# Kernel tuning notes

Measured on AMD Instinct MI355X. Metric: run time of the kernel, lower is better.

The kernel has to match this reference:

```python
import jax, jax.numpy as jnp
import numpy as np
import math

INPUT_SIZE = 1024
OUTPUT_SIZE = 1024
QK_SIZE = 1024
B, S = 4, 2048


def setup_inputs() -> dict:
    key = jax.random.key(0)
    ks = jax.random.split(key, 7)
    scale = 1.0 / math.sqrt(INPUT_SIZE)
    return {
        "x": jax.random.normal(ks[0], (B, S, INPUT_SIZE), dtype=jnp.float32),
        "Wq": jax.random.uniform(ks[1], (QK_SIZE, INPUT_SIZE), minval=-scale, maxval=scale, dtype=jnp.float32),
        "bq": jax.random.uniform(ks[2], (QK_SIZE,), minval=-scale, maxval=scale, dtype=jnp.float32),
        "Wk": jax.random.uniform(ks[3], (QK_SIZE, INPUT_SIZE), minval=-scale, maxval=scale, dtype=jnp.float32),
        "bk": jax.random.uniform(ks[4], (QK_SIZE,), minval=-scale, maxval=scale, dtype=jnp.float32),
        "Wv": jax.random.uniform(ks[5], (OUTPUT_SIZE, INPUT_SIZE), minval=-scale, maxval=scale, dtype=jnp.float32),
        "bv": jax.random.uniform(ks[6], (OUTPUT_SIZE,), minval=-scale, maxval=scale, dtype=jnp.float32),
    }


def reference(x, Wq, bq, Wk, bk, Wv, bv):
    # torch Linear: y = x @ W.T + b
    q = jnp.einsum('bsd,ed->bse', x, Wq) + bq  # [B,S,QK]
    k = jnp.einsum('bsd,ed->bse', x, Wk) + bk  # [B,S,QK]
    v = jnp.einsum('bsd,ed->bse', x, Wv) + bv  # [B,S,OUT]
    inv_sqrt_d = 1.0 / math.sqrt(QK_SIZE)
    scores = jnp.einsum('bqe,bke->bqk', q, k) * inv_sqrt_d  # [B,S,S]
    attn = jax.nn.softmax(scores, axis=-1)
    return jnp.einsum('bqk,bko->bqo', attn, v)  # [B,S,OUT]
```

## Files before the change

kernel.cpp:

```cpp
#include <hip/hip_runtime.h>
#include <stdint.h>

typedef unsigned short u16;
typedef __attribute__((ext_vector_type(8))) __bf16 bf16x8;
typedef __attribute__((ext_vector_type(4))) float f32x4;

__device__ __forceinline__ u16 f2bf(float f) {
    union { float f; uint32_t u; } v; v.f = f;
    uint32_t r = (v.u + 0x7FFFu + ((v.u >> 16) & 1u)) >> 16;
    return (u16)r;
}

__device__ __forceinline__ void lds_fence() {
    __asm__ volatile("s_waitcnt lgkmcnt(0)" ::: "memory");
}

#define BM 128
#define BN 128
#define BK 64

template<int MODE>
__global__ __launch_bounds__(256, 4) void gemm_bt(
    const u16* __restrict__ A, const u16* __restrict__ Bt,
    const float* __restrict__ b0, const float* __restrict__ b1, const float* __restrict__ b2,
    u16* __restrict__ o0, u16* __restrict__ o1, u16* __restrict__ o2,
    float* __restrict__ o3, float* __restrict__ lsum,
    int M, int N, int K, long sA, long sB, long sC, float scale)
{
    __shared__ __align__(16) u16 smem[4 * 64 * 72];

    const int t = threadIdx.x;
    const int lane = t & 63;
    const int wave = t >> 6;
    const int wm = (wave & 1) * 64;
    const int wn = (wave >> 1) * 64;

    const int id = blockIdx.x;
    const int xcd = id & 7;
    const int s = id >> 3;
    int bm, bn;
    long bz;
    if (MODE == 0) {
        bn = (s >> 3) * BN;
        bm = (xcd * 8 + (s & 7)) * BM;
        bz = 0;
    } else if (MODE == 2) {
        bz = xcd >> 1;
        bn = (s & 15) * BN;
        bm = ((xcd & 1) * 8 + (s >> 4)) * BM;
    } else {
        bz = xcd >> 1;
        bn = (s & 7) * BN;
        bm = ((xcd & 1) * 8 + (s >> 3)) * BM;
    }

    const u16* Ab = A + bz * sA;
    const u16* Bb = Bt + bz * sB;

    f32x4 acc[4][4];
#pragma unroll
    for (int i = 0; i < 4; ++i)
#pragma unroll
        for (int j = 0; j < 4; ++j)
            acc[i][j] = (f32x4){0.f, 0.f, 0.f, 0.f};

    const int lrow = t >> 2;
    const int lcol = (t & 3) * 8;
    const int fm = lane & 15;
    const int fk = (lane >> 4) * 8;

    for (int k0 = 0; k0 < K; k0 += BK) {
#pragma unroll
        for (int h = 0; h < 2; ++h)
#pragma unroll
            for (int r = 0; r < 2; ++r) {
                const u16* ga = Ab + (long)(bm + r * 64 + lrow) * K + (k0 + h * 32 + lcol);
                __builtin_amdgcn_global_load_lds(
                    (const __attribute__((address_space(1))) void*)ga,
                    (__attribute__((address_space(3))) void*)&smem[h * 4096 + (r * 256 + t) * 8],
                    16, 0, 0);
            }
#pragma unroll
        for (int h = 0; h < 2; ++h)
#pragma unroll
            for (int r = 0; r < 2; ++r) {
                const u16* gb = Bb + (long)(bn + r * 64 + lrow) * K + (k0 + h * 32 + lcol);
                __builtin_amdgcn_global_load_lds(
                    (const __attribute__((address_space(1))) void*)gb,
                    (__attribute__((address_space(3))) void*)&smem[8192 + h * 4096 + (r * 256 + t) * 8],
                    16, 0, 0);
            }
        __syncthreads();

#pragma unroll
        for (int h = 0; h < 2; ++h) {
            bf16x8 af[4], bfr[4];
#pragma unroll
            for (int i = 0; i < 4; ++i) {
                af[i]  = *(const bf16x8*)&smem[h * 4096 + (wm + i * 16 + fm) * 32 + fk];
                bfr[i] = *(const bf16x8*)&smem[8192 + h * 4096 + (wn + i * 16 + fm) * 32 + fk];
            }
#pragma unroll
            for (int i = 0; i < 4; ++i)
#pragma unroll
                for (int j = 0; j < 4; ++j)
                    acc[i][j] = __builtin_amdgcn_mfma_f32_16x16x32_bf16(af[i], bfr[j], acc[i][j], 0, 0, 0);
        }
        __syncthreads();
    }

    const int cm = (lane >> 4) * 4;
    const int cn = lane & 15;
    u16* Ew = smem + wave * 4608;

    if (MODE == 3) {
        float* Fw = (float*)Ew;
#pragma unroll
        for (int p = 0; p < 2; ++p) {
            if (p) lds_fence();
#pragma unroll
            for (int ii = 0; ii < 2; ++ii) {
                const int i = p * 2 + ii;
#pragma unroll
                for (int j = 0; j < 4; ++j)
#pragma unroll
                    for (int r = 0; r < 4; ++r)
                        Fw[(ii * 16 + cm + r) * 68 + j * 16 + cn] = acc[i][j][r];
            }
#pragma unroll
            for (int it = 0; it < 8; ++it) {
                const int row = it * 4 + (lane >> 4);
                const int c4 = (lane & 15) * 4;
                f32x4 w = *(const f32x4*)&Fw[row * 68 + c4];
                const int gm = bm + wm + p * 32 + row;
                const float inv = __builtin_amdgcn_rcpf(lsum[bz * 2048 + gm]);
                w[0] *= inv; w[1] *= inv; w[2] *= inv; w[3] *= inv;
                *(f32x4*)&o3[bz * sC + (long)gm * N + bn + wn + c4] = w;
            }
        }
    } else if (MODE == 0 && (bn >> 10) == 2) {
        float bb[4];
#pragma unroll
        for (int j = 0; j < 4; ++j) bb[j] = b2[(bn & 1023) + wn + j * 16 + cn];
        const int bgi = (bm + wm) >> 11;
        const int sbase = (bm + wm) & 2047;
#pragma unroll
        for (int i = 0; i < 4; ++i)
#pragma unroll
            for (int j = 0; j < 4; ++j) {
                ushort4 pk;
                pk.x = f2bf(acc[i][j][0] + bb[j]);
                pk.y = f2bf(acc[i][j][1] + bb[j]);
                pk.z = f2bf(acc[i][j][2] + bb[j]);
                pk.w = f2bf(acc[i][j][3] + bb[j]);
                *(ushort4*)&Ew[(j * 16 + cn) * 72 + i * 16 + cm] = pk;
            }
#pragma unroll
        for (int it = 0; it < 8; ++it) {
            const int e = it * 8 + (lane >> 3);
            const int s8 = (lane & 7) * 8;
            const uint4 w = *(const uint4*)&Ew[e * 72 + s8];
            const int eg = (bn & 1023) + wn + e;
            *(uint4*)&o2[((((long)bgi << 10) + eg) << 11) + sbase + s8] = w;
        }
    } else if (MODE == 0) {
        const int sec = bn >> 10;
        u16* C = sec ? o1 : o0;
        const float* bias = sec ? b1 : b0;
        const int ncol0 = bn & 1023;
        float bb[4];
#pragma unroll
        for (int j = 0; j < 4; ++j) bb[j] = bias[ncol0 + wn + j * 16 + cn];
#pragma unroll
        for (int i = 0; i < 4; ++i)
#pragma unroll
            for (int j = 0; j < 4; ++j) {
                const int col = j * 16 + cn;
#pragma unroll
                for (int r = 0; r < 4; ++r)
                    Ew[(i * 16 + cm + r) * 72 + col] = f2bf(acc[i][j][r] + bb[j]);
            }
#pragma unroll
        for (int it = 0; it < 8; ++it) {
            const int row = it * 8 + (lane >> 3);
            const int c8 = (lane & 7) * 8;
            const uint4 w = *(const uint4*)&Ew[row * 72 + c8];
            const int gm = bm + wm + row;
            *(uint4*)&C[(long)gm * 1024 + ncol0 + wn + c8] = w;
        }
    } else {
#pragma unroll
        for (int i = 0; i < 4; ++i)
#pragma unroll
            for (int j = 0; j < 4; ++j)
#pragma unroll
                for (int r = 0; r < 4; ++r)
                    acc[i][j][r] = __expf(acc[i][j][r] * scale);
#pragma unroll
        for (int i = 0; i < 4; ++i) {
#pragma unroll
            for (int r = 0; r < 4; ++r) {
                float sm = acc[i][0][r] + acc[i][1][r] + acc[i][2][r] + acc[i][3][r];
                sm += __shfl_xor(sm, 1);
                sm += __shfl_xor(sm, 2);
                sm += __shfl_xor(sm, 4);
                sm += __shfl_xor(sm, 8);
                if (cn == 0)
                    atomicAdd(&lsum[bz * 2048 + bm + wm + i * 16 + cm + r], sm);
            }
        }
#pragma unroll
        for (int i = 0; i < 4; ++i)
#pragma unroll
            for (int j = 0; j < 4; ++j) {
                const int col = j * 16 + cn;
#pragma unroll
                for (int r = 0; r < 4; ++r)
                    Ew[(i * 16 + cm + r) * 72 + col] = f2bf(acc[i][j][r]);
            }
#pragma unroll
        for (int it = 0; it < 8; ++it) {
            const int row = it * 8 + (lane >> 3);
            const int c8 = (lane & 7) * 8;
            const uint4 w = *(const uint4*)&Ew[row * 72 + c8];
            const int gm = bm + wm + row;
            *(uint4*)&o0[bz * sC + (long)gm * N + bn + wn + c8] = w;
        }
    }
}

__global__ __launch_bounds__(256) void cvt_all(
    const float* __restrict__ x, const float* __restrict__ wq,
    const float* __restrict__ wk, const float* __restrict__ wv,
    u16* __restrict__ xb, u16* __restrict__ wb, float* __restrict__ lsum)
{
    const int b = blockIdx.x;
    if (b >= 11264) {
        const long i = (long)(b - 11264) * 1024 + threadIdx.x * 4;
        *(f32x4*)(lsum + i) = (f32x4){0.f, 0.f, 0.f, 0.f};
        return;
    }
    const float* src; u16* dst; long base;
    if (b < 8192)       { src = x;  dst = xb;             base = (long)b * 1024; }
    else if (b < 9216)  { src = wq; dst = wb;             base = (long)(b - 8192) * 1024; }
    else if (b < 10240) { src = wk; dst = wb + (1 << 20); base = (long)(b - 9216) * 1024; }
    else                { src = wv; dst = wb + (2 << 20); base = (long)(b - 10240) * 1024; }
    const long i = base + threadIdx.x * 4;
    const f32x4 f = *(const f32x4*)(src + i);
    ushort4 o;
    o.x = f2bf(f[0]); o.y = f2bf(f[1]); o.z = f2bf(f[2]); o.w = f2bf(f[3]);
    *(ushort4*)(dst + i) = o;
}

extern "C" void kernel_launch(void* const* d_in, const int* in_sizes, int n_in,
                              void* d_out, int out_size, void* d_ws, size_t ws_size,
                              hipStream_t stream) {
    const float* x  = (const float*)d_in[0];
    const float* Wq = (const float*)d_in[1];
    const float* bq = (const float*)d_in[2];
    const float* Wk = (const float*)d_in[3];
    const float* bk = (const float*)d_in[4];
    const float* Wv = (const float*)d_in[5];
    const float* bv = (const float*)d_in[6];
    float* out = (float*)d_out;

    const int B = 4, S = 2048, D = 1024, E = 1024;
    const int M = B * S;

    u16* xb  = (u16*)d_ws;
    u16* wb  = xb  + (size_t)M * D;
    u16* qb  = wb  + (size_t)3 * E * D;
    u16* kb  = qb  + (size_t)M * E;
    u16* vbT = kb  + (size_t)M * E;
    u16* sb  = vbT + (size_t)M * E;
    float* lsum = (float*)(sb + (size_t)M * S);

    cvt_all<<<11272, 256, 0, stream>>>(x, Wq, Wk, Wv, xb, wb, lsum);

    dim3 blk(256);
    gemm_bt<0><<<1536, blk, 0, stream>>>(
        xb, wb, bq, bk, bv, qb, kb, vbT, nullptr, nullptr, M, 3 * E, D, 0, 0, 0, 1.f);
    gemm_bt<2><<<1024, blk, 0, stream>>>(
        qb, kb, nullptr, nullptr, nullptr, sb, nullptr, nullptr, nullptr, lsum,
        S, S, E, (long)S * E, (long)S * E, (long)S * S, 0.03125f);
    gemm_bt<3><<<512, blk, 0, stream>>>(
        sb, vbT, nullptr, nullptr, nullptr, nullptr, nullptr, nullptr, out, lsum,
        S, E, S, (long)S * S, (long)E * S, (long)S * E, 1.f);
}
```

Before: 232.7 us.

## Rewrite GEMMs as 256x256-tile, 8-wave, double-buffered pipelined kernel with swizzled LDS

Replaces the 128x128 single-buffered GEMM with a 256x256 tile computed by 8 waves (512 threads), using 128KB dynamic LDS with double buffering. Global-to-LDS loads for the next K slices are interleaved with MFMA quadrants through explicit barriers, vmcnt waits and setprio. An XOR swizzle is applied to the LDS column layout to reduce bank conflicts. The larger tiles raise data reuse and cut the grid to 384/256/128 blocks, which fewer than 256 CUs can only partly fill for the last two GEMMs and leaves little occupancy headroom.

```diff
diff --git a/kernel.cpp b/kernel.cpp
--- a/kernel.cpp
+++ b/kernel.cpp
@@ -15,25 +15,25 @@
     __asm__ volatile("s_waitcnt lgkmcnt(0)" ::: "memory");
 }
 
-#define BM 128
-#define BN 128
-#define BK 64
+#define BARRIER() __asm__ volatile("s_barrier" ::: "memory")
+#define VMW(N)    __asm__ volatile("s_waitcnt vmcnt(" #N ")" ::: "memory")
+#define SCHEDB()  __builtin_amdgcn_sched_barrier(0)
 
 template<int MODE>
-__global__ __launch_bounds__(256, 4) void gemm_bt(
+__global__ __launch_bounds__(512, 2) void gemm8(
     const u16* __restrict__ A, const u16* __restrict__ Bt,
     const float* __restrict__ b0, const float* __restrict__ b1, const float* __restrict__ b2,
     u16* __restrict__ o0, u16* __restrict__ o1, u16* __restrict__ o2,
     float* __restrict__ o3, float* __restrict__ lsum,
     int M, int N, int K, long sA, long sB, long sC, float scale)
 {
-    __shared__ __align__(16) u16 smem[4 * 64 * 72];
+    extern __shared__ __align__(16) u16 smem[];
 
     const int t = threadIdx.x;
     const int lane = t & 63;
     const int wave = t >> 6;
-    const int wm = (wave & 1) * 64;
-    const int wn = (wave >> 1) * 64;
+    const int wm = wave >> 2;
+    const int wn = wave & 3;
 
     const int id = blockIdx.x;
     const int xcd = id & 7;
@@ -41,193 +41,268 @@
     int bm, bn;
     long bz;
     if (MODE == 0) {
-        bn = (s >> 3) * BN;
-        bm = (xcd * 8 + (s & 7)) * BM;
+        bm = (xcd * 4 + (s & 3)) * 256;
+        bn = (s >> 2) * 256;
         bz = 0;
     } else if (MODE == 2) {
         bz = xcd >> 1;
-        bn = (s & 15) * BN;
-        bm = ((xcd & 1) * 8 + (s >> 4)) * BM;
+        bm = ((xcd & 1) * 4 + (s & 3)) * 256;
+        bn = (s >> 2) * 256;
     } else {
         bz = xcd >> 1;
-        bn = (s & 7) * BN;
-        bm = ((xcd & 1) * 8 + (s >> 3)) * BM;
+        bm = ((xcd & 1) * 4 + (s & 3)) * 256;
+        bn = (s >> 2) * 256;
     }
 
     const u16* Ab = A + bz * sA;
     const u16* Bb = Bt + bz * sB;
 
-    f32x4 acc[4][4];
-#pragma unroll
-    for (int i = 0; i < 4; ++i)
+    f32x4 acc[8][4];
+#pragma unroll
+    for (int i = 0; i < 8; ++i)
 #pragma unroll
         for (int j = 0; j < 4; ++j)
             acc[i][j] = (f32x4){0.f, 0.f, 0.f, 0.f};
 
-    const int lrow = t >> 2;
-    const int lcol = (t & 3) * 8;
+    const int trow = t >> 2;
+    const int gcol = ((t & 3) * 8) ^ ((trow & 8) << 1);
+    const u16* aRow = Ab + (long)(bm + trow) * K + gcol;
+    const u16* bRow = Bb + (long)(bn + trow) * K + gcol;
+
+    auto stage = [&](int buf, int kt, int h, int isB) {
+        const u16* g = (isB ? bRow : aRow) + (long)(h * 128) * K + kt * 64;
+        u16* d = smem + t * 8 + buf * 32768 + isB * 16384 + h * 8192;
+#pragma unroll
+        for (int l = 0; l < 2; ++l)
+            __builtin_amdgcn_global_load_lds(
+                (const __attribute__((address_space(1))) void*)(g + l * 32),
+                (__attribute__((address_space(3))) void*)(d + l * 4096), 16, 0, 0);
+    };
+
     const int fm = lane & 15;
-    const int fk = (lane >> 4) * 8;
-
-    for (int k0 = 0; k0 < K; k0 += BK) {
-#pragma unroll
-        for (int h = 0; h < 2; ++h)
-#pragma unroll
-            for (int r = 0; r < 2; ++r) {
-                const u16* ga = Ab + (long)(bm + r * 64 + lrow) * K + (k0 + h * 32 + lcol);
-                __builtin_amdgcn_global_load_lds(
-                    (const __attribute__((address_space(1))) void*)ga,
-                    (__attribute__((address_space(3))) void*)&smem[h * 4096 + (r * 256 + t) * 8],
-                    16, 0, 0);
-            }
-#pragma unroll
-        for (int h = 0; h < 2; ++h)
-#pragma unroll
-            for (int r = 0; r < 2; ++r) {
-                const u16* gb = Bb + (long)(bn + r * 64 + lrow) * K + (k0 + h * 32 + lcol);
-                __builtin_amdgcn_global_load_lds(
-                    (const __attribute__((address_space(1))) void*)gb,
-                    (__attribute__((address_space(3))) void*)&smem[8192 + h * 4096 + (r * 256 + t) * 8],
-                    16, 0, 0);
-            }
-        __syncthreads();
-
-#pragma unroll
-        for (int h = 0; h < 2; ++h) {
-            bf16x8 af[4], bfr[4];
-#pragma unroll
-            for (int i = 0; i < 4; ++i) {
-                af[i]  = *(const bf16x8*)&smem[h * 4096 + (wm + i * 16 + fm) * 32 + fk];
-                bfr[i] = *(const bf16x8*)&smem[8192 + h * 4096 + (wn + i * 16 + fm) * 32 + fk];
-            }
-#pragma unroll
-            for (int i = 0; i < 4; ++i)
-#pragma unroll
-                for (int j = 0; j < 4; ++j)
-                    acc[i][j] = __builtin_amdgcn_mfma_f32_16x16x32_bf16(af[i], bfr[j], acc[i][j], 0, 0, 0);
-        }
-        __syncthreads();
-    }
+    const int fcol = ((lane >> 4) * 8) ^ ((fm & 8) << 1);
+    const int aB = wm * 8192 + fm * 32 + fcol;
+    const int bB = 16384 + (wn >> 1) * 8192 + (wn & 1) * 2048 + fm * 32 + fcol;
+
+    bf16x8 fa[4][2], fb0[2][2], fb1[2][2];
+
+#define RD_A(BUF, MH) do { \
+    _Pragma("unroll") for (int mi = 0; mi < 4; ++mi) \
+    _Pragma("unroll") for (int kh = 0; kh < 2; ++kh) \
+        fa[mi][kh] = *(const bf16x8*)&smem[(BUF)*32768 + aB + kh*4096 + (MH)*2048 + mi*512]; \
+} while (0)
+
+#define RD_B(BUF, NH, DST) do { \
+    _Pragma("unroll") for (int ni = 0; ni < 2; ++ni) \
+    _Pragma("unroll") for (int kh = 0; kh < 2; ++kh) \
+        DST[ni][kh] = *(const bf16x8*)&smem[(BUF)*32768 + bB + kh*4096 + (NH)*1024 + ni*512]; \
+} while (0)
+
+#define QUAD(MH, NH, FB) do { \
+    __builtin_amdgcn_s_setprio(1); \
+    _Pragma("unroll") for (int mi = 0; mi < 4; ++mi) \
+    _Pragma("unroll") for (int ni = 0; ni < 2; ++ni) \
+    _Pragma("unroll") for (int kh = 0; kh < 2; ++kh) \
+        acc[(MH)*4+mi][(NH)*2+ni] = __builtin_amdgcn_mfma_f32_16x16x32_bf16( \
+            fa[mi][kh], FB[ni][kh], acc[(MH)*4+mi][(NH)*2+ni], 0, 0, 0); \
+    __builtin_amdgcn_s_setprio(0); \
+} while (0)
+
+    const int NT = K >> 6;
+    const int NI = NT >> 1;
+
+    stage(0, 0, 0, 0); stage(0, 0, 1, 0); stage(0, 0, 0, 1); stage(0, 0, 1, 1);
+    stage(1, 1, 0, 1); stage(1, 1, 0, 0);
+    VMW(4);
+    BARRIER();
+
+    for (int i = 0; i < NI; ++i) {
+        const int knext = 2 * i + 1;
+        int ktc = 2 * i + 2; if (ktc >= NT) ktc -= NT;
+        const int ktd = ktc + 1;
+
+        RD_A(0, 0); RD_B(0, 0, fb0);
+        stage(1, knext, 1, 0);
+        BARRIER(); SCHEDB();
+        QUAD(0, 0, fb0);
+        BARRIER();
+        RD_B(0, 1, fb1);
+        stage(1, knext, 1, 1);
+        BARRIER(); SCHEDB();
+        QUAD(0, 1, fb1);
+        BARRIER();
+        RD_A(0, 1);
+        stage(0, ktc, 0, 1);
+        BARRIER(); SCHEDB();
+        QUAD(1, 1, fb1);
+        BARRIER();
+        stage(0, ktc, 0, 0);
+        BARRIER(); SCHEDB();
+        QUAD(1, 0, fb0);
+        VMW(4);
+        BARRIER();
+        RD_A(1, 0); RD_B(1, 0, fb0);
+        stage(0, ktc, 1, 0);
+        BARRIER(); SCHEDB();
+        QUAD(0, 0, fb0);
+        BARRIER();
+        RD_B(1, 1, fb1);
+        stage(0, ktc, 1, 1);
+        BARRIER(); SCHEDB();
+        QUAD(0, 1, fb1);
+        BARRIER();
+        RD_A(1, 1);
+        stage(1, ktd, 0, 1);
+        BARRIER(); SCHEDB();
+        QUAD(1, 1, fb1);
+        BARRIER();
+        stage(1, ktd, 0, 0);
+        BARRIER(); SCHEDB();
+        QUAD(1, 0, fb0);
+        VMW(4);
+        BARRIER();
+    }
+
+    VMW(0);
+    BARRIER();
 
     const int cm = (lane >> 4) * 4;
     const int cn = lane & 15;
-    u16* Ew = smem + wave * 4608;
+    u16* Ew = smem + wave * 8192;
+    const int gmb = bm + wm * 128;
+    const int cnb = bn + wn * 64;
 
     if (MODE == 3) {
         float* Fw = (float*)Ew;
 #pragma unroll
+        for (int p = 0; p < 4; ++p) {
+            if (p) lds_fence();
+#pragma unroll
+            for (int m2 = 0; m2 < 2; ++m2) {
+                const int mi = p * 2 + m2;
+#pragma unroll
+                for (int ni = 0; ni < 4; ++ni)
+#pragma unroll
+                    for (int r = 0; r < 4; ++r)
+                        Fw[(m2 * 16 + cm + r) * 68 + ni * 16 + cn] = acc[mi][ni][r];
+            }
+#pragma unroll
+            for (int it = 0; it < 8; ++it) {
+                const int row = it * 4 + (lane >> 4);
+                const int c4 = cn * 4;
+                f32x4 w = *(const f32x4*)&Fw[row * 68 + c4];
+                const int gm = gmb + p * 32 + row;
+                const float inv = __builtin_amdgcn_rcpf(lsum[bz * 2048 + gm]);
+                w[0] *= inv; w[1] *= inv; w[2] *= inv; w[3] *= inv;
+                *(f32x4*)&o3[bz * sC + (long)gm * N + cnb + c4] = w;
+            }
+        }
+    } else if (MODE == 0 && (bn >> 10) == 2) {
+        const int ebase = (bn & 1023) + wn * 64;
+        float bb[4];
+#pragma unroll
+        for (int ni = 0; ni < 4; ++ni) bb[ni] = b2[ebase + ni * 16 + cn];
+        const long bgi = gmb >> 11;
+        const int sbase = gmb & 2047;
+#pragma unroll
         for (int p = 0; p < 2; ++p) {
             if (p) lds_fence();
 #pragma unroll
-            for (int ii = 0; ii < 2; ++ii) {
-                const int i = p * 2 + ii;
-#pragma unroll
-                for (int j = 0; j < 4; ++j)
-#pragma unroll
-                    for (int r = 0; r < 4; ++r)
-                        Fw[(ii * 16 + cm + r) * 68 + j * 16 + cn] = acc[i][j][r];
+            for (int m4 = 0; m4 < 4; ++m4) {
+                const int mi = p * 4 + m4;
+#pragma unroll
+                for (int ni = 0; ni < 4; ++ni) {
+                    ushort4 pk;
+                    pk.x = f2bf(acc[mi][ni][0] + bb[ni]);
+                    pk.y = f2bf(acc[mi][ni][1] + bb[ni]);
+                    pk.z = f2bf(acc[mi][ni][2] + bb[ni]);
+                    pk.w = f2bf(acc[mi][ni][3] + bb[ni]);
+                    *(ushort4*)&Ew[(ni * 16 + cn) * 72 + m4 * 16 + cm] = pk;
+                }
             }
 #pragma unroll
             for (int it = 0; it < 8; ++it) {
-                const int row = it * 4 + (lane >> 4);
-                const int c4 = (lane & 15) * 4;
-                f32x4 w = *(const f32x4*)&Fw[row * 68 + c4];
-                const int gm = bm + wm + p * 32 + row;
-                const float inv = __builtin_amdgcn_rcpf(lsum[bz * 2048 + gm]);
-                w[0] *= inv; w[1] *= inv; w[2] *= inv; w[3] *= inv;
-                *(f32x4*)&o3[bz * sC + (long)gm * N + bn + wn + c4] = w;
-            }
-        }
-    } else if (MODE == 0 && (bn >> 10) == 2) {
-        float bb[4];
-#pragma unroll
-        for (int j = 0; j < 4; ++j) bb[j] = b2[(bn & 1023) + wn + j * 16 + cn];
-        const int bgi = (bm + wm) >> 11;
-        const int sbase = (bm + wm) & 2047;
-#pragma unroll
-        for (int i = 0; i < 4; ++i)
-#pragma unroll
-            for (int j = 0; j < 4; ++j) {
-                ushort4 pk;
-                pk.x = f2bf(acc[i][j][0] + bb[j]);
-                pk.y = f2bf(acc[i][j][1] + bb[j]);
-                pk.z = f2bf(acc[i][j][2] + bb[j]);
-                pk.w = f2bf(acc[i][j][3] + bb[j]);
-                *(ushort4*)&Ew[(j * 16 + cn) * 72 + i * 16 + cm] = pk;
-            }
-#pragma unroll
-        for (int it = 0; it < 8; ++it) {
-            const int e = it * 8 + (lane >> 3);
-            const int s8 = (lane & 7) * 8;
-            const uint4 w = *(const uint4*)&Ew[e * 72 + s8];
-            const int eg = (bn & 1023) + wn + e;
-            *(uint4*)&o2[((((long)bgi << 10) + eg) << 11) + sbase + s8] = w;
+                const int e = it * 8 + (lane >> 3);
+                const int s8 = (lane & 7) * 8;
+                const uint4 w = *(const uint4*)&Ew[e * 72 + s8];
+                *(uint4*)&o2[(((bgi << 10) + ebase + e) << 11) + sbase + p * 64 + s8] = w;
+            }
         }
     } else if (MODE == 0) {
         const int sec = bn >> 10;
         u16* C = sec ? o1 : o0;
         const float* bias = sec ? b1 : b0;
-        const int ncol0 = bn & 1023;
+        const int ncol0 = (bn & 1023) + wn * 64;
         float bb[4];
 #pragma unroll
-        for (int j = 0; j < 4; ++j) bb[j] = bias[ncol0 + wn + j * 16 + cn];
-#pragma unroll
-        for (int i = 0; i < 4; ++i)
-#pragma unroll
-            for (int j = 0; j < 4; ++j) {
-                const int col = j * 16 + cn;
+        for (int ni = 0; ni < 4; ++ni) bb[ni] = bias[ncol0 + ni * 16 + cn];
+#pragma unroll
+        for (int p = 0; p < 2; ++p) {
+            if (p) lds_fence();
+#pragma unroll
+            for (int m4 = 0; m4 < 4; ++m4) {
+                const int mi = p * 4 + m4;
+#pragma unroll
+                for (int ni = 0; ni < 4; ++ni)
+#pragma unroll
+                    for (int r = 0; r < 4; ++r)
+                        Ew[(m4 * 16 + cm + r) * 72 + ni * 16 + cn] = f2bf(acc[mi][ni][r] + bb[ni]);
+            }
+#pragma unroll
+            for (int it = 0; it < 8; ++it) {
+                const int row = it * 8 + (lane >> 3);
+                const int c8 = (lane & 7) * 8;
+                const uint4 w = *(const uint4*)&Ew[row * 72 + c8];
+                *(uint4*)&C[(long)(gmb + p * 64 + row) * 1024 + ncol0 + c8] = w;
+            }
+        }
+    } else {
+#pragma unroll
+        for (int mi = 0; mi < 8; ++mi)
+#pragma unroll
+            for (int ni = 0; ni < 4; ++ni)
 #pragma unroll
                 for (int r = 0; r < 4; ++r)
-                    Ew[(i * 16 + cm + r) * 72 + col] = f2bf(acc[i][j][r] + bb[j]);
-            }
-#pragma unroll
-        for (int it = 0; it < 8; ++it) {
-            const int row = it * 8 + (lane >> 3);
-            const int c8 = (lane & 7) * 8;
-            const uint4 w = *(const uint4*)&Ew[row * 72 + c8];
-            const int gm = bm + wm + row;
-            *(uint4*)&C[(long)gm * 1024 + ncol0 + wn + c8] = w;
-        }
-    } else {
-#pragma unroll
-        for (int i = 0; i < 4; ++i)
-#pragma unroll
-            for (int j = 0; j < 4; ++j)
-#pragma unroll
-                for (int r = 0; r < 4; ++r)
-                    acc[i][j][r] = __expf(acc[i][j][r] * scale);
-#pragma unroll
-        for (int i = 0; i < 4; ++i) {
+                    acc[mi][ni][r] = __expf(acc[mi][ni][r] * scale);
+#pragma unroll
+        for (int mi = 0; mi < 8; ++mi) {
 #pragma unroll
             for (int r = 0; r < 4; ++r) {
-                float sm = acc[i][0][r] + acc[i][1][r] + acc[i][2][r] + acc[i][3][r];
+                float sm = acc[mi][0][r] + acc[mi][1][r] + acc[mi][2][r] + acc[mi][3][r];
                 sm += __shfl_xor(sm, 1);
                 sm += __shfl_xor(sm, 2);
                 sm += __shfl_xor(sm, 4);
                 sm += __shfl_xor(sm, 8);
                 if (cn == 0)
-                    atomicAdd(&lsum[bz * 2048 + bm + wm + i * 16 + cm + r], sm);
-            }
-        }
-#pragma unroll
-        for (int i = 0; i < 4; ++i)
-#pragma unroll
-            for (int j = 0; j < 4; ++j) {
-                const int col = j * 16 + cn;
-#pragma unroll
-                for (int r = 0; r < 4; ++r)
-                    Ew[(i * 16 + cm + r) * 72 + col] = f2bf(acc[i][j][r]);
-            }
-#pragma unroll
-        for (int it = 0; it < 8; ++it) {
-            const int row = it * 8 + (lane >> 3);
-            const int c8 = (lane & 7) * 8;
-            const uint4 w = *(const uint4*)&Ew[row * 72 + c8];
-            const int gm = bm + wm + row;
-            *(uint4*)&o0[bz * sC + (long)gm * N + bn + wn + c8] = w;
-        }
-    }
-}
+                    atomicAdd(&lsum[bz * 2048 + gmb + mi * 16 + cm + r], sm);
+            }
+        }
+#pragma unroll
+        for (int p = 0; p < 2; ++p) {
+            if (p) lds_fence();
+#pragma unroll
+            for (int m4 = 0; m4 < 4; ++m4) {
+                const int mi = p * 4 + m4;
+#pragma unroll
+                for (int ni = 0; ni < 4; ++ni)
+#pragma unroll
+                    for (int r = 0; r < 4; ++r)
+                        Ew[(m4 * 16 + cm + r) * 72 + ni * 16 + cn] = f2bf(acc[mi][ni][r]);
+            }
+#pragma unroll
+            for (int it = 0; it < 8; ++it) {
+                const int row = it * 8 + (lane >> 3);
+                const int c8 = (lane & 7) * 8;
+                const uint4 w = *(const uint4*)&Ew[row * 72 + c8];
+                *(uint4*)&o0[bz * sC + (long)(gmb + p * 64 + row) * N + cnb + c8] = w;
+            }
+        }
+    }
+}
+
+#undef RD_A
+#undef RD_B
+#undef QUAD
 
 __global__ __launch_bounds__(256) void cvt_all(
     const float* __restrict__ x, const float* __restrict__ wq,
@@ -266,6 +341,7 @@
 
     const int B = 4, S = 2048, D = 1024, E = 1024;
     const int M = B * S;
+    const size_t LDS = 131072;
 
     u16* xb  = (u16*)d_ws;
     u16* wb  = xb  + (size_t)M * D;
@@ -275,15 +351,23 @@
     u16* sb  = vbT + (size_t)M * E;
     float* lsum = (float*)(sb + (size_t)M * S);
 
+    static bool attr_done = false;
+    if (!attr_done) {
+        (void)hipFuncSetAttribute((const void*)gemm8<0>, hipFuncAttributeMaxDynamicSharedMemorySize, (int)LDS);
+        (void)hipFuncSetAttribute((const void*)gemm8<2>, hipFuncAttributeMaxDynamicSharedMemorySize, (int)LDS);
+        (void)hipFuncSetAttribute((const void*)gemm8<3>, hipFuncAttributeMaxDynamicSharedMemorySize, (int)LDS);
+        attr_done = true;
+    }
+
     cvt_all<<<11272, 256, 0, stream>>>(x, Wq, Wk, Wv, xb, wb, lsum);
 
-    dim3 blk(256);
-    gemm_bt<0><<<1536, blk, 0, stream>>>(
+    dim3 blk(512);
+    gemm8<0><<<384, blk, LDS, stream>>>(
         xb, wb, bq, bk, bv, qb, kb, vbT, nullptr, nullptr, M, 3 * E, D, 0, 0, 0, 1.f);
-    gemm_bt<2><<<1024, blk, 0, stream>>>(
+    gemm8<2><<<256, blk, LDS, stream>>>(
         qb, kb, nullptr, nullptr, nullptr, sb, nullptr, nullptr, nullptr, lsum,
         S, S, E, (long)S * E, (long)S * E, (long)S * S, 0.03125f);
-    gemm_bt<3><<<512, blk, 0, stream>>>(
+    gemm8<3><<<128, blk, LDS, stream>>>(
         sb, vbT, nullptr, nullptr, nullptr, nullptr, nullptr, nullptr, out, lsum,
         S, E, S, (long)S * S, (long)E * S, (long)S * E, 1.f);
 }
```

After: 244.0 us. 4.9% more time.

## Fuse all stages into one persistent kernel with grid barriers and atomic work queues

Applied to the files above, without the earlier changes.

Replaces four separate launches (convert, QKV GEMM, scores GEMM, PV GEMM) with one persistent kernel of 1024 blocks. Stages are separated by software grid barriers, and tiles are handed out through per-XCD atomic counters. The softmax row-sum atomics are replaced by per-column-slot partial sums that the final stage reduces itself, which also removes the lsum zeroing pass. The goal is to remove launch gaps and tail effects, at the cost of spin-wait barriers, a co-residency assumption for 1024 blocks, and a timeout break that could silently produce wrong results.

```diff
diff --git a/kernel.cpp b/kernel.cpp
--- a/kernel.cpp
+++ b/kernel.cpp
@@ -19,23 +19,36 @@
 #define BN 128
 #define BK 64
 
+
+__device__ __forceinline__ void grid_bar(uint* cnt, uint target, int t) {
+    __syncthreads();
+    if (t == 0) {
+        __hip_atomic_fetch_add(cnt, 1u, __ATOMIC_RELEASE, __HIP_MEMORY_SCOPE_AGENT);
+        uint g = 0;
+        while (__hip_atomic_load(cnt, __ATOMIC_RELAXED, __HIP_MEMORY_SCOPE_AGENT) < target) {
+            __builtin_amdgcn_s_sleep(2);
+            if (++g > (1u << 22)) break;
+        }
+        __builtin_amdgcn_fence(__ATOMIC_ACQUIRE, "agent");
+    }
+    __syncthreads();
+}
+
 template<int MODE>
-__global__ __launch_bounds__(256, 4) void gemm_bt(
+__device__ __forceinline__ void tile_body(
+    int id, u16* smem,
     const u16* __restrict__ A, const u16* __restrict__ Bt,
     const float* __restrict__ b0, const float* __restrict__ b1, const float* __restrict__ b2,
     u16* __restrict__ o0, u16* __restrict__ o1, u16* __restrict__ o2,
-    float* __restrict__ o3, float* __restrict__ lsum,
-    int M, int N, int K, long sA, long sB, long sC, float scale)
+    float* __restrict__ o3, float* __restrict__ psum,
+    int N, int K, long sA, long sB, long sC, float scale)
 {
-    __shared__ __align__(16) u16 smem[4 * 64 * 72];
-
     const int t = threadIdx.x;
     const int lane = t & 63;
     const int wave = t >> 6;
     const int wm = (wave & 1) * 64;
     const int wn = (wave >> 1) * 64;
 
-    const int id = blockIdx.x;
     const int xcd = id & 7;
     const int s = id >> 3;
     int bm, bn;
@@ -114,6 +127,15 @@
     u16* Ew = smem + wave * 4608;
 
     if (MODE == 3) {
+        float* denom = (float*)((char*)smem + 8704);
+        if (t < 128) {
+            float d = 0.f;
+#pragma unroll
+            for (int j = 0; j < 32; ++j)
+                d += psum[(bz * 32 + j) * 2048 + bm + t];
+            denom[t] = d;
+        }
+        __syncthreads();
         float* Fw = (float*)Ew;
 #pragma unroll
         for (int p = 0; p < 2; ++p) {
@@ -132,10 +154,10 @@
                 const int row = it * 4 + (lane >> 4);
                 const int c4 = (lane & 15) * 4;
                 f32x4 w = *(const f32x4*)&Fw[row * 68 + c4];
-                const int gm = bm + wm + p * 32 + row;
-                const float inv = __builtin_amdgcn_rcpf(lsum[bz * 2048 + gm]);
+                const int lr = wm + p * 32 + row;
+                const float inv = __builtin_amdgcn_rcpf(denom[lr]);
                 w[0] *= inv; w[1] *= inv; w[2] *= inv; w[3] *= inv;
-                *(f32x4*)&o3[bz * sC + (long)gm * N + bn + wn + c4] = w;
+                *(f32x4*)&o3[bz * sC + (long)(bm + lr) * N + bn + wn + c4] = w;
             }
         }
     } else if (MODE == 0 && (bn >> 10) == 2) {
@@ -196,6 +218,7 @@
 #pragma unroll
                 for (int r = 0; r < 4; ++r)
                     acc[i][j][r] = __expf(acc[i][j][r] * scale);
+        const int slot = (bn >> 7) * 2 + (wn >> 6);
 #pragma unroll
         for (int i = 0; i < 4; ++i) {
 #pragma unroll
@@ -206,7 +229,7 @@
                 sm += __shfl_xor(sm, 4);
                 sm += __shfl_xor(sm, 8);
                 if (cn == 0)
-                    atomicAdd(&lsum[bz * 2048 + bm + wm + i * 16 + cm + r], sm);
+                    psum[(bz * 32 + slot) * 2048 + bm + wm + i * 16 + cm + r] = sm;
             }
         }
 #pragma unroll
@@ -229,27 +252,73 @@
     }
 }
 
-__global__ __launch_bounds__(256) void cvt_all(
-    const float* __restrict__ x, const float* __restrict__ wq,
-    const float* __restrict__ wk, const float* __restrict__ wv,
-    u16* __restrict__ xb, u16* __restrict__ wb, float* __restrict__ lsum)
+__global__ __launch_bounds__(256, 4) void fused_attn(
+    const float* __restrict__ x,
+    const float* __restrict__ Wq, const float* __restrict__ bq,
+    const float* __restrict__ Wk, const float* __restrict__ bk,
+    const float* __restrict__ Wv, const float* __restrict__ bv,
+    u16* xb, u16* wb, u16* qb, u16* kb, u16* vbT, u16* sb,
+    float* psum, float* out, uint* sync)
 {
+    __shared__ __align__(16) u16 smem[4 * 64 * 72];
+    __shared__ uint widx;
+
     const int b = blockIdx.x;
-    if (b >= 11264) {
-        const long i = (long)(b - 11264) * 1024 + threadIdx.x * 4;
-        *(f32x4*)(lsum + i) = (f32x4){0.f, 0.f, 0.f, 0.f};
-        return;
-    }
-    const float* src; u16* dst; long base;
-    if (b < 8192)       { src = x;  dst = xb;             base = (long)b * 1024; }
-    else if (b < 9216)  { src = wq; dst = wb;             base = (long)(b - 8192) * 1024; }
-    else if (b < 10240) { src = wk; dst = wb + (1 << 20); base = (long)(b - 9216) * 1024; }
-    else                { src = wv; dst = wb + (2 << 20); base = (long)(b - 10240) * 1024; }
-    const long i = base + threadIdx.x * 4;
-    const f32x4 f = *(const f32x4*)(src + i);
-    ushort4 o;
-    o.x = f2bf(f[0]); o.y = f2bf(f[1]); o.z = f2bf(f[2]); o.w = f2bf(f[3]);
-    *(ushort4*)(dst + i) = o;
+    const int t = threadIdx.x;
+    const int xcd = b & 7;
+
+#pragma unroll
+    for (int j = 0; j < 11; ++j) {
+        const int bb = b + (j << 10);
+        const float* src; u16* dst; long base;
+        if (bb < 8192)       { src = x;  dst = xb;             base = (long)bb << 10; }
+        else if (bb < 9216)  { src = Wq; dst = wb;             base = (long)(bb - 8192) << 10; }
+        else if (bb < 10240) { src = Wk; dst = wb + (1 << 20); base = (long)(bb - 9216) << 10; }
+        else                 { src = Wv; dst = wb + (2 << 20); base = (long)(bb - 10240) << 10; }
+        const long i = base + t * 4;
+        const f32x4 f = *(const f32x4*)(src + i);
+        ushort4 o;
+        o.x = f2bf(f[0]); o.y = f2bf(f[1]); o.z = f2bf(f[2]); o.w = f2bf(f[3]);
+        *(ushort4*)(dst + i) = o;
+    }
+    grid_bar(sync, 1024, t);
+
+    for (;;) {
+        __syncthreads();
+        if (t == 0) widx = __hip_atomic_fetch_add(&sync[8 + xcd], 1u,
+                             __ATOMIC_RELAXED, __HIP_MEMORY_SCOPE_AGENT);
+        __syncthreads();
+        const uint i = widx;
+        if (i >= 192) break;
+        tile_body<0>(xcd + 8 * (int)i, smem, xb, wb, bq, bk, bv, qb, kb, vbT,
+                     nullptr, nullptr, 3072, 1024, 0, 0, 0, 1.f);
+    }
+    grid_bar(sync, 2048, t);
+
+    for (;;) {
+        __syncthreads();
+        if (t == 0) widx = __hip_atomic_fetch_add(&sync[16 + xcd], 1u,
+                             __ATOMIC_RELAXED, __HIP_MEMORY_SCOPE_AGENT);
+        __syncthreads();
+        const uint i = widx;
+        if (i >= 128) break;
+        tile_body<2>(xcd + 8 * (int)i, smem, qb, kb, nullptr, nullptr, nullptr,
+                     sb, nullptr, nullptr, nullptr, psum, 2048, 1024,
+                     (long)2048 * 1024, (long)2048 * 1024, (long)2048 * 2048, 0.03125f);
+    }
+    grid_bar(sync, 3072, t);
+
+    for (;;) {
+        __syncthreads();
+        if (t == 0) widx = __hip_atomic_fetch_add(&sync[24 + xcd], 1u,
+                             __ATOMIC_RELAXED, __HIP_MEMORY_SCOPE_AGENT);
+        __syncthreads();
+        const uint i = widx;
+        if (i >= 64) break;
+        tile_body<3>(xcd + 8 * (int)i, smem, sb, vbT, nullptr, nullptr, nullptr,
+                     nullptr, nullptr, nullptr, out, psum, 1024, 2048,
+                     (long)2048 * 2048, (long)1024 * 2048, (long)2048 * 1024, 1.f);
+    }
 }
 
 extern "C" void kernel_launch(void* const* d_in, const int* in_sizes, int n_in,
@@ -273,17 +342,10 @@
     u16* kb  = qb  + (size_t)M * E;
     u16* vbT = kb  + (size_t)M * E;
     u16* sb  = vbT + (size_t)M * E;
-    float* lsum = (float*)(sb + (size_t)M * S);
-
-    cvt_all<<<11272, 256, 0, stream>>>(x, Wq, Wk, Wv, xb, wb, lsum);
-
-    dim3 blk(256);
-    gemm_bt<0><<<1536, blk, 0, stream>>>(
-        xb, wb, bq, bk, bv, qb, kb, vbT, nullptr, nullptr, M, 3 * E, D, 0, 0, 0, 1.f);
-    gemm_bt<2><<<1024, blk, 0, stream>>>(
-        qb, kb, nullptr, nullptr, nullptr, sb, nullptr, nullptr, nullptr, lsum,
-        S, S, E, (long)S * E, (long)S * E, (long)S * S, 0.03125f);
-    gemm_bt<3><<<512, blk, 0, stream>>>(
-        sb, vbT, nullptr, nullptr, nullptr, nullptr, nullptr, nullptr, out, lsum,
-        S, E, S, (long)S * S, (long)E * S, (long)S * E, 1.f);
-}
+    float* psum = (float*)(sb + (size_t)M * S);
+    uint* sync  = (uint*)(psum + (size_t)4 * 32 * 2048);
+
+    hipMemsetAsync(sync, 0, 128, stream);
+    fused_attn<<<1024, 256, 0, stream>>>(
+        x, Wq, bq, Wk, bk, Wv, bv, xb, wb, qb, kb, vbT, sb, psum, out, sync);
+}
```

After: 710.4 us. 205% more time.
